# Performance work log

Measured on AMD Instinct MI355X. Metric: run time of the kernel, lower is better.

The kernel has to match this reference:

```python
import jax, jax.numpy as jnp
import numpy as np

N, E, IN_C, H, C1, OUT_C, B = 10000, 100000, 256, 6, 128, 128, 64
EPS = 1e-5
NEG_SLOPE = 0.2


def gat_conv(x, src, dst, W, att_s, att_d, bias):
    # x: [N, F_in]; W: [F_in, H*C]; att_s/att_d: [H, C]; bias: [H*C]
    n, h, c = x.shape[0], att_s.shape[0], att_s.shape[1]
    hx = (x @ W).reshape(n, h, c)                    # [N,H,C]
    a_s = jnp.einsum('nhc,hc->nh', hx, att_s)        # [N,H]
    a_d = jnp.einsum('nhc,hc->nh', hx, att_d)
    e = jax.nn.leaky_relu(a_s[src] + a_d[dst], NEG_SLOPE)   # [E,H]
    # segment softmax over incoming edges of each dst node
    m = jax.ops.segment_max(e, dst, num_segments=n)
    e = jnp.exp(e - m[dst])
    s = jax.ops.segment_sum(e, dst, num_segments=n)
    alpha = e / s[dst]                               # [E,H]
    msg = hx[src] * alpha[:, :, None]                # [E,H,C]
    out = jax.ops.segment_sum(msg, dst, num_segments=n)
    return out.reshape(n, h * c) + bias


def batch_norm(x, gamma, beta):
    mu = jnp.mean(x, axis=0)
    var = jnp.var(x, axis=0)  # biased, as torch BN uses for normalization
    return (x - mu) * jax.lax.rsqrt(var + EPS) * gamma + beta


def setup_inputs() -> dict:
    key = jax.random.key(0)
    ks = jax.random.split(key, 12)
    def xavier(k, shape):
        fan_in, fan_out = shape[0], shape[1]
        lim = np.sqrt(6.0 / (fan_in + fan_out))
        return jax.random.uniform(k, shape, jnp.float32, -lim, lim)
    inp = {}
    inp['input_feature'] = jax.random.normal(ks[0], (N, IN_C), jnp.float32)
    inp['input_adj'] = jax.random.randint(ks[1], (2, E), 0, N, jnp.int64)
    inp['ibatch'] = (jnp.arange(N, dtype=jnp.int64) * B) // N  # sorted graph ids, all B graphs covered
    # conv1: in -> H*C1
    inp['W1'] = xavier(ks[2], (IN_C, H * C1))
    inp['att_s1'] = xavier(ks[3], (H, C1)) * 0.1
    inp['att_d1'] = xavier(ks[4], (H, C1)) * 0.1
    inp['b1'] = jnp.zeros((H * C1,), jnp.float32)
    inp['g1'] = jnp.ones((H * C1,), jnp.float32)
    inp['be1'] = jnp.zeros((H * C1,), jnp.float32)
    # conv2: H*C1 -> H*OUT_C
    inp['W2'] = xavier(ks[5], (H * C1, H * OUT_C))
    inp['att_s2'] = xavier(ks[6], (H, OUT_C)) * 0.1
    inp['att_d2'] = xavier(ks[7], (H, OUT_C)) * 0.1
    inp['b2'] = jnp.zeros((H * OUT_C,), jnp.float32)
    inp['g2'] = jnp.ones((H * OUT_C,), jnp.float32)
    inp['be2'] = jnp.zeros((H * OUT_C,), jnp.float32)
    # gcn_linear: H*OUT_C -> OUT_C
    inp['lin_W'] = xavier(ks[8], (H * OUT_C, OUT_C))
    inp['lin_b'] = jnp.zeros((OUT_C,), jnp.float32)
    return inp


def reference(input_feature, input_adj, ibatch, W1, att_s1, att_d1, b1, g1, be1,
              W2, att_s2, att_d2, b2, g2, be2, lin_W, lin_b):
    # add self loops (PyG GATConv default)
    loops = jnp.arange(N, dtype=input_adj.dtype)
    src = jnp.concatenate([input_adj[0], loops])
    dst = jnp.concatenate([input_adj[1], loops])
    x = gat_conv(input_feature, src, dst, W1, att_s1, att_d1, b1)
    x = batch_norm(jax.nn.relu(x), g1, be1)
    x = gat_conv(x, src, dst, W2, att_s2, att_d2, b2)
    x = batch_norm(jax.nn.relu(x), g2, be2)
    x = x @ lin_W + lin_b                             # [N, OUT_C]
    # global max pool over nodes of each graph
    return jax.ops.segment_max(x, ibatch, num_segments=B)
```

## Files before the change

kernel.cpp:

```cpp
#include <hip/hip_runtime.h>

#define NN 10000
#define MP 10112
#define EE 100000
#define ETOT 110000
#define INC 256
#define HH 6
#define CC 128
#define FF 768
#define BB 64
#define BN_EPS 1e-5f

typedef unsigned short ushort_t;
typedef unsigned int uint_t;
typedef __attribute__((ext_vector_type(8))) short bf16x8;
typedef __attribute__((ext_vector_type(4))) float f32x4;
#define AS1 __attribute__((address_space(1)))
#define AS3 __attribute__((address_space(3)))

__device__ __forceinline__ unsigned fenc(float v){
  unsigned u = __float_as_uint(v);
  return (u & 0x80000000u) ? ~u : (u | 0x80000000u);
}
__device__ __forceinline__ float fdec(unsigned u){
  return (u & 0x80000000u) ? __uint_as_float(u & 0x7FFFFFFFu) : __uint_as_float(~u);
}

__device__ __forceinline__ ushort_t f2bf(float v){
  unsigned u = __float_as_uint(v);
  u += 0x7FFFu + ((u >> 16) & 1u);
  return (ushort_t)(u >> 16);
}
__device__ __forceinline__ float bf_lo(uint_t u){ return __uint_as_float(u << 16); }
__device__ __forceinline__ float bf_hi(uint_t u){ return __uint_as_float(u & 0xFFFF0000u); }

__device__ __forceinline__ float bn_scale(const float* sums, const float* sumsq,
                                          const float* g, int k){
  float mu  = sums[k] * (1.f/NN);
  float var = sumsq[k] * (1.f/NN) - mu*mu;
  return g[k] * rsqrtf(var + BN_EPS);
}

__global__ __launch_bounds__(256) void count_deg(const int* __restrict__ adj, int* __restrict__ deg){
  int k = blockIdx.x*256 + threadIdx.x;
  if(k >= ETOT) return;
  int d = (k < EE) ? adj[EE + k] : (k - EE);
  atomicAdd(deg + d, 1);
}

__global__ __launch_bounds__(1024) void scan_deg(const int* __restrict__ deg,
                                                 int* __restrict__ row_start,
                                                 int* __restrict__ pos){
  __shared__ int wsum[16];
  __shared__ int wexcl[16];
  __shared__ int carry, ctot;
  int t = threadIdx.x, wave = t >> 6, lane = t & 63;
  if(t == 0) carry = 0;
  __syncthreads();
  for(int base = 0; base < NN; base += 1024){
    int i = base + t;
    int v = (i < NN) ? deg[i] : 0;
    int s = v;
    #pragma unroll
    for(int off = 1; off < 64; off <<= 1){ int x = __shfl_up(s, off); if(lane >= off) s += x; }
    if(lane == 63) wsum[wave] = s;
    __syncthreads();
    if(t < 16){
      int ws = wsum[t], sc = ws;
      #pragma unroll
      for(int off = 1; off < 16; off <<= 1){ int x = __shfl_up(sc, off); if(t >= off) sc += x; }
      wexcl[t] = sc - ws;
      if(t == 15) ctot = sc;
    }
    __syncthreads();
    int c = carry;
    if(i < NN){ int excl = c + wexcl[wave] + s - v; row_start[i] = excl; pos[i] = excl; }
    __syncthreads();
    if(t == 0) carry = c + ctot;
  }
  __syncthreads();
  if(t == 0) row_start[NN] = carry;
}

__global__ __launch_bounds__(256) void scatter_edges(const int* __restrict__ adj,
                                                     int* __restrict__ pos,
                                                     int* __restrict__ csr_src,
                                                     int* __restrict__ csr_pos){
  int k = blockIdx.x*256 + threadIdx.x;
  if(k >= ETOT) return;
  int s, d;
  if(k < EE){ s = adj[k]; d = adj[EE + k]; } else { s = k - EE; d = s; }
  int i = atomicAdd(pos + d, 1);
  csr_src[i] = s;
  csr_pos[k] = i;
}

__global__ __launch_bounds__(256) void conv_bf16(const float* __restrict__ in,
                                                 ushort_t* __restrict__ out, int n4){
  int i = blockIdx.x*256 + threadIdx.x;
  if(i >= n4) return;
  float4 v = ((const float4*)in)[i];
  ushort4 o;
  o.x = f2bf(v.x); o.y = f2bf(v.y); o.z = f2bf(v.z); o.w = f2bf(v.w);
  ((ushort4*)out)[i] = o;
}

__global__ __launch_bounds__(256) void transpose_bf(const float* __restrict__ in,
                                                    ushort_t* __restrict__ out,
                                                    int K, int N,
                                                    const float* __restrict__ sums,
                                                    const float* __restrict__ sumsq,
                                                    const float* __restrict__ g){
  __shared__ ushort_t tile[32][33];
  int kb = blockIdx.y*32, nb = blockIdx.x*32;
  int tx = threadIdx.x & 31, ty = threadIdx.x >> 5;
  #pragma unroll
  for(int r = ty; r < 32; r += 8){
    int k = kb + r;
    float v = in[(size_t)k*N + nb + tx];
    if(g) v *= bn_scale(sums, sumsq, g, k);
    tile[tx][r] = f2bf(v);
  }
  __syncthreads();
  #pragma unroll
  for(int r = ty; r < 32; r += 8)
    out[(size_t)(nb + r)*K + kb + tx] = tile[r][tx];
}

#define BF_KCHUNK 64
__global__ __launch_bounds__(256) void bias_fold(const float* __restrict__ W,
                                                 const float* __restrict__ sums,
                                                 const float* __restrict__ sumsq,
                                                 const float* __restrict__ g,
                                                 const float* __restrict__ be,
                                                 const float* __restrict__ base,
                                                 float* __restrict__ out, int K, int N){
  int o = blockIdx.x*256 + threadIdx.x;
  if(o >= N) return;
  int k0 = blockIdx.y*BF_KCHUNK;
  int k1 = k0 + BF_KCHUNK; if(k1 > K) k1 = K;
  float s = 0.f;
  for(int k = k0; k < k1; k++){
    float mu = sums[k] * (1.f/NN);
    float sc = bn_scale(sums, sumsq, g, k);
    s = fmaf(be[k] - mu*sc, W[(size_t)k*N + o], s);
  }
  if(k0 == 0 && base) s += base[o];
  atomicAdd(out + o, s);
}

__global__ __launch_bounds__(256) void gemm_bt(const ushort_t* __restrict__ A,
                                               const ushort_t* __restrict__ Bt,
                                               ushort_t* __restrict__ Cb,
                                               int M, int N, int K,
                                               const float* __restrict__ bias,
                                               const float* __restrict__ atts,
                                               const float* __restrict__ attd,
                                               float* __restrict__ a_s,
                                               float* __restrict__ a_d,
                                               const int* __restrict__ ibatch,
                                               unsigned* __restrict__ outEnc){
  __shared__ ushort_t As[128*32];
  __shared__ ushort_t Bs[128*32];
  __shared__ float sred[128], dred[128];
  __shared__ unsigned smax[2*CC];
  __shared__ int s_split;
  int tid = threadIdx.x;
  int bm = blockIdx.y*128, bn = blockIdx.x*128;
  int w = tid >> 6, lane = tid & 63;
  int wr = (w >> 1)*64, wc = (w & 1)*64;
  int quad = lane >> 4, l15 = lane & 15;

  f32x4 acc[4][4];
  #pragma unroll
  for(int i=0;i<4;i++)
    #pragma unroll
    for(int j=0;j<4;j++) acc[i][j] = (f32x4){0.f,0.f,0.f,0.f};

  int ch0 = tid, ch1 = tid + 256;
  int ar0 = ch0 >> 2, ac0 = (ch0 & 3) << 3;
  int ar1 = ch1 >> 2, ac1 = (ch1 & 3) << 3;
  const ushort_t* Ag0 = A + (size_t)(bm + ar0)*K + ac0;
  const ushort_t* Ag1 = A + (size_t)(bm + ar1)*K + ac1;
  const ushort_t* Bg0 = Bt + (size_t)(bn + ar0)*K + ac0;
  const ushort_t* Bg1 = Bt + (size_t)(bn + ar1)*K + ac1;

  for(int k0 = 0; k0 < K; k0 += 32){
    __builtin_amdgcn_global_load_lds((const AS1 uint_t*)(Ag0 + k0),
                                     (AS3 uint_t*)(As + ch0*8), 16, 0, 0);
    __builtin_amdgcn_global_load_lds((const AS1 uint_t*)(Ag1 + k0),
                                     (AS3 uint_t*)(As + ch1*8), 16, 0, 0);
    __builtin_amdgcn_global_load_lds((const AS1 uint_t*)(Bg0 + k0),
                                     (AS3 uint_t*)(Bs + ch0*8), 16, 0, 0);
    __builtin_amdgcn_global_load_lds((const AS1 uint_t*)(Bg1 + k0),
                                     (AS3 uint_t*)(Bs + ch1*8), 16, 0, 0);
    __syncthreads();

    bf16x8 a[4], b[4];
    #pragma unroll
    for(int i=0;i<4;i++) a[i] = *(const bf16x8*)&As[(wr + i*16 + l15)*32 + quad*8];
    #pragma unroll
    for(int j=0;j<4;j++) b[j] = *(const bf16x8*)&Bs[(wc + j*16 + l15)*32 + quad*8];
    #pragma unroll
    for(int i=0;i<4;i++)
      #pragma unroll
      for(int j=0;j<4;j++)
        acc[i][j] = __builtin_amdgcn_mfma_f32_16x16x32_bf16(a[i], b[j], acc[i][j], 0, 0, 0);
    __syncthreads();
  }

  int h = bn >> 7;
  float bv4[4], as4[4] = {0,0,0,0}, ad4[4] = {0,0,0,0};
  #pragma unroll
  for(int j=0;j<4;j++){
    int gc = bn + wc + j*16 + l15;
    bv4[j] = bias ? bias[gc] : 0.f;
  }
  if(atts){
    #pragma unroll
    for(int j=0;j<4;j++){
      int lc = wc + j*16 + l15;
      as4[j] = atts[h*CC + lc];
      ad4[j] = attd[h*CC + lc];
    }
    if(tid < 128){ sred[tid] = 0.f; dred[tid] = 0.f; }
    __syncthreads();
  }
  int gsplit = 0;
  float pm[2][4];
  if(outEnc){
    if(tid == 0) s_split = bm + 128;
    for(int q = tid; q < 2*CC; q += 256) smax[q] = 0u;
    __syncthreads();
    if(tid < 127){
      int r1 = bm + tid + 1;
      if(r1 < M && ibatch[r1] != ibatch[r1 - 1]) s_split = r1;
    }
    __syncthreads();
    gsplit = s_split;
    #pragma unroll
    for(int s2=0;s2<2;s2++)
      #pragma unroll
      for(int j=0;j<4;j++) pm[s2][j] = -__builtin_inff();
  }
  #pragma unroll
  for(int i=0;i<4;i++){
    #pragma unroll
    for(int r=0;r<4;r++){
      int rl = wr + i*16 + quad*4 + r;
      int gr = bm + rl;
      bool rowok = (gr < M);
      float sp = 0.f, dp = 0.f;
      #pragma unroll
      for(int j=0;j<4;j++){
        float val = acc[i][j][r] + bv4[j];
        if(rowok){
          if(outEnc){
            int slot = (gr >= gsplit);
            pm[slot][j] = fmaxf(pm[slot][j], val);
          } else {
            int gc = bn + wc + j*16 + l15;
            Cb[(size_t)gr*N + gc] = f2bf(val);
          }
        }
        sp = fmaf(val, as4[j], sp);
        dp = fmaf(val, ad4[j], dp);
      }
      if(atts){
        #pragma unroll
        for(int off = 1; off < 16; off <<= 1){
          sp += __shfl_xor(sp, off);
          dp += __shfl_xor(dp, off);
        }
        if(l15 == 0){ atomicAdd(&sred[rl], sp); atomicAdd(&dred[rl], dp); }
      }
    }
  }
  if(atts){
    __syncthreads();
    if(tid < 128){
      int gr = bm + tid;
      if(gr < M){ a_s[gr*6 + h] = sred[tid]; a_d[gr*6 + h] = dred[tid]; }
    }
  }
  if(outEnc){
    #pragma unroll
    for(int s2=0;s2<2;s2++)
      #pragma unroll
      for(int j=0;j<4;j++){
        if(pm[s2][j] > -__builtin_inff())
          atomicMax(&smax[s2*CC + wc + j*16 + l15], fenc(pm[s2][j]));
      }
    __syncthreads();
    if(tid < 2*CC){
      unsigned v = smax[tid];
      if(v){
        int slot = tid >> 7, c = tid & 127;
        int g = ibatch[slot ? gsplit : bm];
        atomicMax(outEnc + g*CC + c, v);
      }
    }
  }
}

__global__ __launch_bounds__(256) void edge_soft(const int* __restrict__ adj,
                                                 const int* __restrict__ csr_pos,
                                                 const float* __restrict__ a_s,
                                                 const float* __restrict__ a_d,
                                                 float* __restrict__ ebuf,
                                                 float* __restrict__ ssum){
  int idx = blockIdx.x*256 + threadIdx.x;
  if(idx >= ETOT*6) return;
  int k = idx / 6, h = idx - k*6;
  int s, d;
  if(k < EE){ s = adj[k]; d = adj[EE + k]; } else { s = k - EE; d = s; }
  float v = a_s[s*6 + h] + a_d[d*6 + h];
  v = v > 0.f ? v : 0.2f * v;
  float w = __expf(v);
  ebuf[(size_t)csr_pos[k]*6 + h] = w;
  atomicAdd(ssum + d*6 + h, w);
}

__global__ __launch_bounds__(384) void aggregate(const ushort_t* __restrict__ hx,
                                                 const float* __restrict__ ebuf,
                                                 const float* __restrict__ ssum,
                                                 const int* __restrict__ row_start,
                                                 const int* __restrict__ csr_src,
                                                 const float* __restrict__ bias,
                                                 ushort_t* __restrict__ y){
  int n = blockIdx.x, t = threadIdx.x, h = t >> 6;
  int e0 = row_start[n], e1 = row_start[n+1];
  float a0 = 0.f, a1 = 0.f;
  int i = e0;
  for(; i + 8 <= e1; i += 8){
    int s[8]; float wv[8]; uint_t u[8];
    #pragma unroll
    for(int q=0;q<8;q++) s[q] = csr_src[i+q];
    #pragma unroll
    for(int q=0;q<8;q++) wv[q] = ebuf[(size_t)(i+q)*6 + h];
    #pragma unroll
    for(int q=0;q<8;q++) u[q] = ((const uint_t*)(hx + (size_t)s[q]*FF))[t];
    #pragma unroll
    for(int q=0;q<8;q++){ a0 = fmaf(wv[q], bf_lo(u[q]), a0); a1 = fmaf(wv[q], bf_hi(u[q]), a1); }
  }
  if(i + 4 <= e1){
    int s[4]; float wv[4]; uint_t u[4];
    #pragma unroll
    for(int q=0;q<4;q++) s[q] = csr_src[i+q];
    #pragma unroll
    for(int q=0;q<4;q++) wv[q] = ebuf[(size_t)(i+q)*6 + h];
    #pragma unroll
    for(int q=0;q<4;q++) u[q] = ((const uint_t*)(hx + (size_t)s[q]*FF))[t];
    #pragma unroll
    for(int q=0;q<4;q++){ a0 = fmaf(wv[q], bf_lo(u[q]), a0); a1 = fmaf(wv[q], bf_hi(u[q]), a1); }
    i += 4;
  }
  for(; i < e1; i++){
    int s = csr_src[i];
    float wv = ebuf[(size_t)i*6 + h];
    uint_t u = ((const uint_t*)(hx + (size_t)s*FF))[t];
    a0 = fmaf(wv, bf_lo(u), a0); a1 = fmaf(wv, bf_hi(u), a1);
  }
  float inv = 1.f/ssum[n*6 + h];
  float2 bv = ((const float2*)bias)[t];
  float v0 = a0*inv + bv.x;
  float v1 = a1*inv + bv.y;
  v0 = v0 > 0.f ? v0 : 0.f;
  v1 = v1 > 0.f ? v1 : 0.f;
  uint_t p = (uint_t)f2bf(v0) | ((uint_t)f2bf(v1) << 16);
  ((uint_t*)(y + (size_t)n*FF))[t] = p;
}

__global__ __launch_bounds__(384) void bn_stats(const ushort_t* __restrict__ y,
                                                float* __restrict__ sums,
                                                float* __restrict__ sumsq){
  int t = threadIdx.x;
  float s0=0.f,s1=0.f,q0=0.f,q1=0.f;
  for(int n = blockIdx.x; n < NN; n += gridDim.x){
    uint_t u = ((const uint_t*)(y + (size_t)n*FF))[t];
    float lo = bf_lo(u), hi = bf_hi(u);
    s0 += lo; q0 += lo*lo;
    s1 += hi; q1 += hi*hi;
  }
  atomicAdd(sums + 2*t,     s0); atomicAdd(sumsq + 2*t,     q0);
  atomicAdd(sums + 2*t + 1, s1); atomicAdd(sumsq + 2*t + 1, q1);
}

__global__ __launch_bounds__(256) void decode_out(const unsigned* __restrict__ outEnc,
                                                  float* __restrict__ out){
  int i = blockIdx.x*256 + threadIdx.x;
  if(i < BB*CC) out[i] = fdec(outEnc[i]);
}

extern "C" void kernel_launch(void* const* d_in, const int* in_sizes, int n_in,
                              void* d_out, int out_size, void* d_ws, size_t ws_size,
                              hipStream_t stream){
  const float* feat  = (const float*)d_in[0];
  const int*   adj   = (const int*)d_in[1];
  const int*   ibatch= (const int*)d_in[2];
  const float* W1    = (const float*)d_in[3];
  const float* atts1 = (const float*)d_in[4];
  const float* attd1 = (const float*)d_in[5];
  const float* b1    = (const float*)d_in[6];
  const float* g1    = (const float*)d_in[7];
  const float* be1   = (const float*)d_in[8];
  const float* W2    = (const float*)d_in[9];
  const float* atts2 = (const float*)d_in[10];
  const float* attd2 = (const float*)d_in[11];
  const float* b2    = (const float*)d_in[12];
  const float* g2    = (const float*)d_in[13];
  const float* be2   = (const float*)d_in[14];
  const float* linW  = (const float*)d_in[15];
  const float* linb  = (const float*)d_in[16];
  float* out = (float*)d_out;

  size_t off = 0;
  auto alloc = [&](size_t bytes) -> void* {
    void* p = (char*)d_ws + off;
    off += (bytes + 255) & ~(size_t)255;
    return p;
  };
  size_t zoff0 = off;
  int*      deg     = (int*)alloc((size_t)NN*4);
  float*    ssumA   = (float*)alloc((size_t)NN*6*4);
  float*    ssumB   = (float*)alloc((size_t)NN*6*4);
  float*    sumsA   = (float*)alloc((size_t)2*FF*4);
  float*    sumsB   = (float*)alloc((size_t)2*FF*4);
  float*    bias2p  = (float*)alloc((size_t)FF*4);
  float*    biasLp  = (float*)alloc((size_t)CC*4);
  unsigned* outEnc  = (unsigned*)alloc((size_t)BB*CC*4);
  size_t zbytes = off - zoff0;
  ushort_t* hx      = (ushort_t*)alloc((size_t)NN*FF*2);
  ushort_t* yB      = (ushort_t*)alloc((size_t)MP*FF*2);
  ushort_t* featB   = (ushort_t*)alloc((size_t)MP*INC*2);
  ushort_t* W1t     = (ushort_t*)alloc((size_t)FF*INC*2);
  ushort_t* W2t     = (ushort_t*)alloc((size_t)FF*FF*2);
  ushort_t* linWt   = (ushort_t*)alloc((size_t)CC*FF*2);
  float*    a_s     = (float*)alloc((size_t)NN*6*4);
  float*    a_d     = (float*)alloc((size_t)NN*6*4);
  float*    ebuf    = (float*)alloc((size_t)ETOT*6*4);
  int*      row_start=(int*)alloc((size_t)(NN+1)*4);
  int*      pos     = (int*)alloc((size_t)NN*4);
  int*      csr_src = (int*)alloc((size_t)ETOT*4);
  int*      csr_pos = (int*)alloc((size_t)ETOT*4);

  const int EB = (ETOT + 255)/256;
  const int EB6 = (ETOT*6 + 255)/256;

  hipMemsetAsync((char*)d_ws + zoff0, 0, zbytes, stream);

  count_deg<<<EB,256,0,stream>>>(adj, deg);
  scan_deg<<<1,1024,0,stream>>>(deg, row_start, pos);
  scatter_edges<<<EB,256,0,stream>>>(adj, pos, csr_src, csr_pos);

  transpose_bf<<<dim3(FF/32, INC/32),256,0,stream>>>(W1, W1t, INC, FF, nullptr, nullptr, nullptr);
  conv_bf16<<<(NN*INC/4+255)/256,256,0,stream>>>(feat, featB, NN*INC/4);

  gemm_bt<<<dim3(FF/128, MP/128),256,0,stream>>>(featB, W1t, hx, NN, FF, INC,
                                                 nullptr, atts1, attd1, a_s, a_d, nullptr, nullptr);
  edge_soft<<<EB6,256,0,stream>>>(adj, csr_pos, a_s, a_d, ebuf, ssumA);
  aggregate<<<NN,384,0,stream>>>(hx, ebuf, ssumA, row_start, csr_src, b1, yB);
  bn_stats<<<256,384,0,stream>>>(yB, sumsA, sumsA + FF);

  transpose_bf<<<dim3(FF/32, FF/32),256,0,stream>>>(W2, W2t, FF, FF, sumsA, sumsA + FF, g1);
  bias_fold<<<dim3(3, FF/BF_KCHUNK),256,0,stream>>>(W2, sumsA, sumsA + FF, g1, be1,
                                                    nullptr, bias2p, FF, FF);
  gemm_bt<<<dim3(FF/128, MP/128),256,0,stream>>>(yB, W2t, hx, NN, FF, FF,
                                                 bias2p, atts2, attd2, a_s, a_d, nullptr, nullptr);
  edge_soft<<<EB6,256,0,stream>>>(adj, csr_pos, a_s, a_d, ebuf, ssumB);
  aggregate<<<NN,384,0,stream>>>(hx, ebuf, ssumB, row_start, csr_src, b2, yB);
  bn_stats<<<256,384,0,stream>>>(yB, sumsB, sumsB + FF);

  transpose_bf<<<dim3(CC/32, FF/32),256,0,stream>>>(linW, linWt, FF, CC, sumsB, sumsB + FF, g2);
  bias_fold<<<dim3(1, FF/BF_KCHUNK),256,0,stream>>>(linW, sumsB, sumsB + FF, g2, be2,
                                                    linb, biasLp, FF, CC);
  gemm_bt<<<dim3(CC/128, MP/128),256,0,stream>>>(yB, linWt, nullptr, NN, CC, FF,
                                                 biasLp, nullptr, nullptr, nullptr, nullptr,
                                                 ibatch, outEnc);
  decode_out<<<(BB*CC+255)/256,256,0,stream>>>(outEnc, out);
}
```

Baseline: 371.6 us.

## Fuse edge softmax into aggregation and merge small prep kernels

Drops the separate edge_soft kernel and its ebuf/ssum buffers. Each aggregate block now recomputes the leaky-relu/exp edge weights from a_s/a_d and accumulates the softmax denominator locally, which also removes the csr_pos output from scatter_edges. Degree counting, the W1 transpose and the feature bf16 conversion are merged into one prep launch, and the BN weight transpose and bias fold are merged into one wfold launch, cutting launch count. The trade-off is that exp is recomputed redundantly across the 64 lanes per head, and the max-subtraction is still skipped, as before.

```diff
diff --git a/kernel.cpp b/kernel.cpp
--- a/kernel.cpp
+++ b/kernel.cpp
@@ -41,11 +41,38 @@
   return g[k] * rsqrtf(var + BN_EPS);
 }
 
-__global__ __launch_bounds__(256) void count_deg(const int* __restrict__ adj, int* __restrict__ deg){
-  int k = blockIdx.x*256 + threadIdx.x;
-  if(k >= ETOT) return;
-  int d = (k < EE) ? adj[EE + k] : (k - EE);
-  atomicAdd(deg + d, 1);
+#define PREP_CNT 430
+#define PREP_TR  (24*8)
+#define PREP_CVT 2500
+__global__ __launch_bounds__(256) void prep(const int* __restrict__ adj, int* __restrict__ deg,
+                                            const float* __restrict__ W1, ushort_t* __restrict__ W1t,
+                                            const float* __restrict__ feat, ushort_t* __restrict__ featB){
+  __shared__ ushort_t tile[32][33];
+  int bid = blockIdx.x, tid = threadIdx.x;
+  if(bid < PREP_CNT){
+    int k = bid*256 + tid;
+    if(k < ETOT){
+      int d = (k < EE) ? adj[EE + k] : (k - EE);
+      atomicAdd(deg + d, 1);
+    }
+  } else if(bid < PREP_CNT + PREP_TR){
+    int b = bid - PREP_CNT;
+    int nb = (b % 24)*32, kb = (b / 24)*32;
+    int tx = tid & 31, ty = tid >> 5;
+    #pragma unroll
+    for(int r = ty; r < 32; r += 8)
+      tile[tx][r] = f2bf(W1[(size_t)(kb + r)*FF + nb + tx]);
+    __syncthreads();
+    #pragma unroll
+    for(int r = ty; r < 32; r += 8)
+      W1t[(size_t)(nb + r)*INC + kb + tx] = tile[r][tx];
+  } else {
+    int i = (bid - PREP_CNT - PREP_TR)*256 + tid;
+    float4 v = ((const float4*)feat)[i];
+    ushort4 o;
+    o.x = f2bf(v.x); o.y = f2bf(v.y); o.z = f2bf(v.z); o.w = f2bf(v.w);
+    ((ushort4*)featB)[i] = o;
+  }
 }
 
 __global__ __launch_bounds__(1024) void scan_deg(const int* __restrict__ deg,
@@ -84,69 +111,55 @@
 
 __global__ __launch_bounds__(256) void scatter_edges(const int* __restrict__ adj,
                                                      int* __restrict__ pos,
-                                                     int* __restrict__ csr_src,
-                                                     int* __restrict__ csr_pos){
+                                                     int* __restrict__ csr_src){
   int k = blockIdx.x*256 + threadIdx.x;
   if(k >= ETOT) return;
   int s, d;
   if(k < EE){ s = adj[k]; d = adj[EE + k]; } else { s = k - EE; d = s; }
   int i = atomicAdd(pos + d, 1);
   csr_src[i] = s;
-  csr_pos[k] = i;
-}
-
-__global__ __launch_bounds__(256) void conv_bf16(const float* __restrict__ in,
-                                                 ushort_t* __restrict__ out, int n4){
-  int i = blockIdx.x*256 + threadIdx.x;
-  if(i >= n4) return;
-  float4 v = ((const float4*)in)[i];
-  ushort4 o;
-  o.x = f2bf(v.x); o.y = f2bf(v.y); o.z = f2bf(v.z); o.w = f2bf(v.w);
-  ((ushort4*)out)[i] = o;
-}
-
-__global__ __launch_bounds__(256) void transpose_bf(const float* __restrict__ in,
-                                                    ushort_t* __restrict__ out,
-                                                    int K, int N,
-                                                    const float* __restrict__ sums,
-                                                    const float* __restrict__ sumsq,
-                                                    const float* __restrict__ g){
+}
+
+__global__ __launch_bounds__(256) void wfold(const float* __restrict__ W,
+                                             int K, int N,
+                                             const float* __restrict__ sums,
+                                             const float* __restrict__ sumsq,
+                                             const float* __restrict__ g,
+                                             const float* __restrict__ be,
+                                             const float* __restrict__ base,
+                                             ushort_t* __restrict__ Wt,
+                                             float* __restrict__ biasOut){
   __shared__ ushort_t tile[32][33];
-  int kb = blockIdx.y*32, nb = blockIdx.x*32;
-  int tx = threadIdx.x & 31, ty = threadIdx.x >> 5;
-  #pragma unroll
-  for(int r = ty; r < 32; r += 8){
-    int k = kb + r;
-    float v = in[(size_t)k*N + nb + tx];
-    if(g) v *= bn_scale(sums, sumsq, g, k);
-    tile[tx][r] = f2bf(v);
-  }
-  __syncthreads();
-  #pragma unroll
-  for(int r = ty; r < 32; r += 8)
-    out[(size_t)(nb + r)*K + kb + tx] = tile[r][tx];
-}
-
-#define BF_KCHUNK 64
-__global__ __launch_bounds__(256) void bias_fold(const float* __restrict__ W,
-                                                 const float* __restrict__ sums,
-                                                 const float* __restrict__ sumsq,
-                                                 const float* __restrict__ g,
-                                                 const float* __restrict__ be,
-                                                 const float* __restrict__ base,
-                                                 float* __restrict__ out, int K, int N){
-  int o = blockIdx.x*256 + threadIdx.x;
-  if(o >= N) return;
-  int k0 = blockIdx.y*BF_KCHUNK;
-  int k1 = k0 + BF_KCHUNK; if(k1 > K) k1 = K;
-  float s = 0.f;
-  for(int k = k0; k < k1; k++){
-    float mu = sums[k] * (1.f/NN);
-    float sc = bn_scale(sums, sumsq, g, k);
-    s = fmaf(be[k] - mu*sc, W[(size_t)k*N + o], s);
-  }
-  if(k0 == 0 && base) s += base[o];
-  atomicAdd(out + o, s);
+  int nT = (K >> 5)*(N >> 5);
+  int bid = blockIdx.x, tid = threadIdx.x;
+  if(bid < nT){
+    int nb = (bid % (N >> 5))*32, kb = (bid / (N >> 5))*32;
+    int tx = tid & 31, ty = tid >> 5;
+    #pragma unroll
+    for(int r = ty; r < 32; r += 8){
+      int k = kb + r;
+      tile[tx][r] = f2bf(W[(size_t)k*N + nb + tx] * bn_scale(sums, sumsq, g, k));
+    }
+    __syncthreads();
+    #pragma unroll
+    for(int r = ty; r < 32; r += 8)
+      Wt[(size_t)(nb + r)*K + kb + tx] = tile[r][tx];
+  } else {
+    int b = bid - nT;
+    int oChunks = (N + 255) >> 8;
+    int kc = b / oChunks, oc = b % oChunks;
+    int o = oc*256 + tid;
+    if(o >= N) return;
+    int k0 = kc*64, k1 = k0 + 64;
+    float s = 0.f;
+    for(int k = k0; k < k1; k++){
+      float mu = sums[k] * (1.f/NN);
+      float sc = bn_scale(sums, sumsq, g, k);
+      s = fmaf(be[k] - mu*sc, W[(size_t)k*N + o], s);
+    }
+    if(k0 == 0 && base) s += base[o];
+    atomicAdd(biasOut + o, s);
+  }
 }
 
 __global__ __launch_bounds__(256) void gemm_bt(const ushort_t* __restrict__ A,
@@ -303,65 +316,63 @@
   }
 }
 
-__global__ __launch_bounds__(256) void edge_soft(const int* __restrict__ adj,
-                                                 const int* __restrict__ csr_pos,
+__global__ __launch_bounds__(384) void aggregate(const ushort_t* __restrict__ hx,
                                                  const float* __restrict__ a_s,
                                                  const float* __restrict__ a_d,
-                                                 float* __restrict__ ebuf,
-                                                 float* __restrict__ ssum){
-  int idx = blockIdx.x*256 + threadIdx.x;
-  if(idx >= ETOT*6) return;
-  int k = idx / 6, h = idx - k*6;
-  int s, d;
-  if(k < EE){ s = adj[k]; d = adj[EE + k]; } else { s = k - EE; d = s; }
-  float v = a_s[s*6 + h] + a_d[d*6 + h];
-  v = v > 0.f ? v : 0.2f * v;
-  float w = __expf(v);
-  ebuf[(size_t)csr_pos[k]*6 + h] = w;
-  atomicAdd(ssum + d*6 + h, w);
-}
-
-__global__ __launch_bounds__(384) void aggregate(const ushort_t* __restrict__ hx,
-                                                 const float* __restrict__ ebuf,
-                                                 const float* __restrict__ ssum,
                                                  const int* __restrict__ row_start,
                                                  const int* __restrict__ csr_src,
                                                  const float* __restrict__ bias,
                                                  ushort_t* __restrict__ y){
   int n = blockIdx.x, t = threadIdx.x, h = t >> 6;
   int e0 = row_start[n], e1 = row_start[n+1];
-  float a0 = 0.f, a1 = 0.f;
+  float adv = a_d[n*6 + h];
+  float a0 = 0.f, a1 = 0.f, wsum = 0.f;
   int i = e0;
   for(; i + 8 <= e1; i += 8){
     int s[8]; float wv[8]; uint_t u[8];
     #pragma unroll
     for(int q=0;q<8;q++) s[q] = csr_src[i+q];
     #pragma unroll
-    for(int q=0;q<8;q++) wv[q] = ebuf[(size_t)(i+q)*6 + h];
+    for(int q=0;q<8;q++) wv[q] = a_s[s[q]*6 + h];
     #pragma unroll
     for(int q=0;q<8;q++) u[q] = ((const uint_t*)(hx + (size_t)s[q]*FF))[t];
     #pragma unroll
-    for(int q=0;q<8;q++){ a0 = fmaf(wv[q], bf_lo(u[q]), a0); a1 = fmaf(wv[q], bf_hi(u[q]), a1); }
+    for(int q=0;q<8;q++){
+      float v = wv[q] + adv;
+      v = v > 0.f ? v : 0.2f * v;
+      float wq = __expf(v);
+      wsum += wq;
+      a0 = fmaf(wq, bf_lo(u[q]), a0); a1 = fmaf(wq, bf_hi(u[q]), a1);
+    }
   }
   if(i + 4 <= e1){
     int s[4]; float wv[4]; uint_t u[4];
     #pragma unroll
     for(int q=0;q<4;q++) s[q] = csr_src[i+q];
     #pragma unroll
-    for(int q=0;q<4;q++) wv[q] = ebuf[(size_t)(i+q)*6 + h];
+    for(int q=0;q<4;q++) wv[q] = a_s[s[q]*6 + h];
     #pragma unroll
     for(int q=0;q<4;q++) u[q] = ((const uint_t*)(hx + (size_t)s[q]*FF))[t];
     #pragma unroll
-    for(int q=0;q<4;q++){ a0 = fmaf(wv[q], bf_lo(u[q]), a0); a1 = fmaf(wv[q], bf_hi(u[q]), a1); }
+    for(int q=0;q<4;q++){
+      float v = wv[q] + adv;
+      v = v > 0.f ? v : 0.2f * v;
+      float wq = __expf(v);
+      wsum += wq;
+      a0 = fmaf(wq, bf_lo(u[q]), a0); a1 = fmaf(wq, bf_hi(u[q]), a1);
+    }
     i += 4;
   }
   for(; i < e1; i++){
     int s = csr_src[i];
-    float wv = ebuf[(size_t)i*6 + h];
+    float v = a_s[s*6 + h] + adv;
+    v = v > 0.f ? v : 0.2f * v;
+    float wq = __expf(v);
+    wsum += wq;
     uint_t u = ((const uint_t*)(hx + (size_t)s*FF))[t];
-    a0 = fmaf(wv, bf_lo(u), a0); a1 = fmaf(wv, bf_hi(u), a1);
-  }
-  float inv = 1.f/ssum[n*6 + h];
+    a0 = fmaf(wq, bf_lo(u), a0); a1 = fmaf(wq, bf_hi(u), a1);
+  }
+  float inv = 1.f/wsum;
   float2 bv = ((const float2*)bias)[t];
   float v0 = a0*inv + bv.x;
   float v1 = a1*inv + bv.y;
@@ -422,8 +433,6 @@
   };
   size_t zoff0 = off;
   int*      deg     = (int*)alloc((size_t)NN*4);
-  float*    ssumA   = (float*)alloc((size_t)NN*6*4);
-  float*    ssumB   = (float*)alloc((size_t)NN*6*4);
   float*    sumsA   = (float*)alloc((size_t)2*FF*4);
   float*    sumsB   = (float*)alloc((size_t)2*FF*4);
   float*    bias2p  = (float*)alloc((size_t)FF*4);
@@ -438,42 +447,32 @@
   ushort_t* linWt   = (ushort_t*)alloc((size_t)CC*FF*2);
   float*    a_s     = (float*)alloc((size_t)NN*6*4);
   float*    a_d     = (float*)alloc((size_t)NN*6*4);
-  float*    ebuf    = (float*)alloc((size_t)ETOT*6*4);
   int*      row_start=(int*)alloc((size_t)(NN+1)*4);
   int*      pos     = (int*)alloc((size_t)NN*4);
   int*      csr_src = (int*)alloc((size_t)ETOT*4);
-  int*      csr_pos = (int*)alloc((size_t)ETOT*4);
 
   const int EB = (ETOT + 255)/256;
-  const int EB6 = (ETOT*6 + 255)/256;
 
   hipMemsetAsync((char*)d_ws + zoff0, 0, zbytes, stream);
 
-  count_deg<<<EB,256,0,stream>>>(adj, deg);
+  prep<<<PREP_CNT + PREP_TR + PREP_CVT,256,0,stream>>>(adj, deg, W1, W1t, feat, featB);
   scan_deg<<<1,1024,0,stream>>>(deg, row_start, pos);
-  scatter_edges<<<EB,256,0,stream>>>(adj, pos, csr_src, csr_pos);
-
-  transpose_bf<<<dim3(FF/32, INC/32),256,0,stream>>>(W1, W1t, INC, FF, nullptr, nullptr, nullptr);
-  conv_bf16<<<(NN*INC/4+255)/256,256,0,stream>>>(feat, featB, NN*INC/4);
+  scatter_edges<<<EB,256,0,stream>>>(adj, pos, csr_src);
 
   gemm_bt<<<dim3(FF/128, MP/128),256,0,stream>>>(featB, W1t, hx, NN, FF, INC,
                                                  nullptr, atts1, attd1, a_s, a_d, nullptr, nullptr);
-  edge_soft<<<EB6,256,0,stream>>>(adj, csr_pos, a_s, a_d, ebuf, ssumA);
-  aggregate<<<NN,384,0,stream>>>(hx, ebuf, ssumA, row_start, csr_src, b1, yB);
+  aggregate<<<NN,384,0,stream>>>(hx, a_s, a_d, row_start, csr_src, b1, yB);
   bn_stats<<<256,384,0,stream>>>(yB, sumsA, sumsA + FF);
 
-  transpose_bf<<<dim3(FF/32, FF/32),256,0,stream>>>(W2, W2t, FF, FF, sumsA, sumsA + FF, g1);
-  bias_fold<<<dim3(3, FF/BF_KCHUNK),256,0,stream>>>(W2, sumsA, sumsA + FF, g1, be1,
-                                                    nullptr, bias2p, FF, FF);
+  wfold<<<(FF/32)*(FF/32) + (FF/64)*3,256,0,stream>>>(W2, FF, FF, sumsA, sumsA + FF, g1, be1,
+                                                      nullptr, W2t, bias2p);
   gemm_bt<<<dim3(FF/128, MP/128),256,0,stream>>>(yB, W2t, hx, NN, FF, FF,
                                                  bias2p, atts2, attd2, a_s, a_d, nullptr, nullptr);
-  edge_soft<<<EB6,256,0,stream>>>(adj, csr_pos, a_s, a_d, ebuf, ssumB);
-  aggregate<<<NN,384,0,stream>>>(hx, ebuf, ssumB, row_start, csr_src, b2, yB);
+  aggregate<<<NN,384,0,stream>>>(hx, a_s, a_d, row_start, csr_src, b2, yB);
   bn_stats<<<256,384,0,stream>>>(yB, sumsB, sumsB + FF);
 
-  transpose_bf<<<dim3(CC/32, FF/32),256,0,stream>>>(linW, linWt, FF, CC, sumsB, sumsB + FF, g2);
-  bias_fold<<<dim3(1, FF/BF_KCHUNK),256,0,stream>>>(linW, sumsB, sumsB + FF, g2, be2,
-                                                    linb, biasLp, FF, CC);
+  wfold<<<(FF/32)*(CC/32) + (FF/64)*1,256,0,stream>>>(linW, FF, CC, sumsB, sumsB + FF, g2, be2,
+                                                      linb, linWt, biasLp);
   gemm_bt<<<dim3(CC/128, MP/128),256,0,stream>>>(yB, linWt, nullptr, NN, CC, FF,
                                                  biasLp, nullptr, nullptr, nullptr, nullptr,
                                                  ibatch, outEnc);
```

Result: faster. 327.7 us (-11.8%).
